# Kernel optimization log

Measured on AMD Instinct MI355X. Metric: run time of the kernel, lower is better.

Reference implementation:

```python
import jax, jax.numpy as jnp
import numpy as np

EPS = 1e-5  # torch.nn.LayerNorm default


def _layer_norm(h, g, b):
    mu = jnp.mean(h, axis=-1, keepdims=True)
    var = jnp.mean(jnp.square(h - mu), axis=-1, keepdims=True)
    return (h - mu) * jax.lax.rsqrt(var + EPS) * g + b


def setup_inputs() -> dict:
    key = jax.random.key(0)
    ks = jax.random.split(key, 16)
    N, E, D, G, H = 100000, 3200000, 16, 64, 8
    x = jax.random.normal(ks[0], (N, D), dtype=jnp.float32)
    edge_index = jax.random.randint(ks[1], (2, E), 0, N, dtype=jnp.int64)
    vp = jax.random.normal(ks[2], (G, D), dtype=jnp.float32)
    batch = jnp.sort(jax.random.randint(ks[3], (N,), 0, G, dtype=jnp.int64))
    def lin(k, fan_in, fan_out):
        bound = 1.0 / np.sqrt(fan_in)
        kw, kb = jax.random.split(k)
        W = jax.random.uniform(kw, (fan_in, fan_out), jnp.float32, -bound, bound)
        b = jax.random.uniform(kb, (fan_out,), jnp.float32, -bound, bound)
        return W, b
    W1, b1 = lin(ks[4], 3 * D, H)
    W2, b2 = lin(ks[5], H, H)
    W3, b3 = lin(ks[6], H, H)
    W4, b4 = lin(ks[7], H, 1)
    g1 = jnp.ones((H,), jnp.float32); be1 = jnp.zeros((H,), jnp.float32)
    g2 = jnp.ones((H,), jnp.float32); be2 = jnp.zeros((H,), jnp.float32)
    g3 = jnp.ones((H,), jnp.float32); be3 = jnp.zeros((H,), jnp.float32)
    return dict(x=x, edge_index=edge_index, vp=vp, batch=batch,
                W1=W1, b1=b1, g1=g1, be1=be1,
                W2=W2, b2=b2, g2=g2, be2=be2,
                W3=W3, b3=b3, g3=g3, be3=be3,
                W4=W4, b4=b4)


def reference(x, edge_index, vp, batch,
              W1, b1, g1, be1, W2, b2, g2, be2, W3, b3, g3, be3, W4, b4):
    start, end = edge_index[0], edge_index[1]
    # gather node features for both endpoints + per-graph features of the start node's event
    edge_inputs = jnp.concatenate([x[start], x[end], vp[batch[start]]], axis=1)  # [E, 3D]
    h = jnp.tanh(_layer_norm(edge_inputs @ W1 + b1, g1, be1))
    h = jnp.tanh(_layer_norm(h @ W2 + b2, g2, be2))
    h = jnp.tanh(_layer_norm(h @ W3 + b3, g3, be3))
    out = h @ W4 + b4  # [E, 1]
    return out.squeeze(-1)
```

## Files before the change

kernel.cpp:

```cpp
#include <hip/hip_runtime.h>


__device__ __forceinline__ float fast_tanh(float v) {
    float e = __expf(2.0f * v);
    return (e - 1.0f) * __builtin_amdgcn_rcpf(e + 1.0f);
}

__device__ __forceinline__ void ln_tanh8(float* h, const float* __restrict__ g,
                                         const float* __restrict__ be) {
    float mu = 0.0f;
#pragma unroll
    for (int j = 0; j < 8; ++j) mu += h[j];
    mu *= 0.125f;
    float var = 0.0f;
#pragma unroll
    for (int j = 0; j < 8; ++j) { float d = h[j] - mu; var += d * d; }
    var *= 0.125f;
    float r = __builtin_amdgcn_rsqf(var + 1e-5f);
#pragma unroll
    for (int j = 0; j < 8; ++j)
        h[j] = fast_tanh((h[j] - mu) * r * g[j] + be[j]);
}

__global__ __launch_bounds__(256) void node_pre_kernel(
    const float* __restrict__ x,
    const int* __restrict__ batch,
    const float* __restrict__ vp,
    const float* __restrict__ W1,
    const float* __restrict__ b1,
    float* __restrict__ y,
    int N)
{
    int n = blockIdx.x * blockDim.x + threadIdx.x;
    if (n >= N) return;

    const float4* px = reinterpret_cast<const float4*>(x) + (size_t)n * 4;
    float4 x0 = px[0], x1 = px[1], x2 = px[2], x3 = px[3];
    int g = batch[n];
    const float4* pv = reinterpret_cast<const float4*>(vp) + (size_t)g * 4;
    float4 v0 = pv[0], v1 = pv[1], v2 = pv[2], v3 = pv[3];

    float xs[16] = {x0.x, x0.y, x0.z, x0.w, x1.x, x1.y, x1.z, x1.w,
                    x2.x, x2.y, x2.z, x2.w, x3.x, x3.y, x3.z, x3.w};
    float vs[16] = {v0.x, v0.y, v0.z, v0.w, v1.x, v1.y, v1.z, v1.w,
                    v2.x, v2.y, v2.z, v2.w, v3.x, v3.y, v3.z, v3.w};

    float ya[8], yb[8];
#pragma unroll
    for (int j = 0; j < 8; ++j) ya[j] = b1[j];
#pragma unroll
    for (int j = 0; j < 8; ++j) yb[j] = 0.0f;

#pragma unroll
    for (int i = 0; i < 16; ++i) {
        float vx = xs[i];
        float vv = vs[i];
#pragma unroll
        for (int j = 0; j < 8; ++j) {
            ya[j] = fmaf(vx, W1[i * 8 + j], ya[j]);
            ya[j] = fmaf(vv, W1[(32 + i) * 8 + j], ya[j]);
            yb[j] = fmaf(vx, W1[(16 + i) * 8 + j], yb[j]);
        }
    }

    float4* py = reinterpret_cast<float4*>(y) + (size_t)n * 4;
    py[0] = make_float4(ya[0], ya[1], ya[2], ya[3]);
    py[1] = make_float4(ya[4], ya[5], ya[6], ya[7]);
    py[2] = make_float4(yb[0], yb[1], yb[2], yb[3]);
    py[3] = make_float4(yb[4], yb[5], yb[6], yb[7]);
}

__global__ __launch_bounds__(256) void edge_main_kernel(
    const int* __restrict__ ei,
    const float* __restrict__ y,
    const float* __restrict__ g1, const float* __restrict__ be1,
    const float* __restrict__ W2, const float* __restrict__ b2,
    const float* __restrict__ g2, const float* __restrict__ be2,
    const float* __restrict__ W3, const float* __restrict__ b3,
    const float* __restrict__ g3, const float* __restrict__ be3,
    const float* __restrict__ W4, const float* __restrict__ b4,
    float* __restrict__ out, int E)
{
    int e = blockIdx.x * blockDim.x + threadIdx.x;
    if (e >= E) return;

    int s = ei[e];
    int t = ei[E + e];

    const float4* pa = reinterpret_cast<const float4*>(y) + (size_t)s * 4;
    const float4* pb = reinterpret_cast<const float4*>(y) + (size_t)t * 4 + 2;
    float4 a0 = pa[0], a1 = pa[1];
    float4 c0 = pb[0], c1 = pb[1];

    float h[8] = {a0.x + c0.x, a0.y + c0.y, a0.z + c0.z, a0.w + c0.w,
                  a1.x + c1.x, a1.y + c1.y, a1.z + c1.z, a1.w + c1.w};
    ln_tanh8(h, g1, be1);

    float h2[8];
#pragma unroll
    for (int j = 0; j < 8; ++j) h2[j] = b2[j];
#pragma unroll
    for (int i = 0; i < 8; ++i) {
        float v = h[i];
#pragma unroll
        for (int j = 0; j < 8; ++j) h2[j] = fmaf(v, W2[i * 8 + j], h2[j]);
    }
    ln_tanh8(h2, g2, be2);

    float h3[8];
#pragma unroll
    for (int j = 0; j < 8; ++j) h3[j] = b3[j];
#pragma unroll
    for (int i = 0; i < 8; ++i) {
        float v = h2[i];
#pragma unroll
        for (int j = 0; j < 8; ++j) h3[j] = fmaf(v, W3[i * 8 + j], h3[j]);
    }
    ln_tanh8(h3, g3, be3);

    float o = b4[0];
#pragma unroll
    for (int i = 0; i < 8; ++i) o = fmaf(h3[i], W4[i], o);

    out[e] = o;
}

__global__ __launch_bounds__(256) void edge_net_fallback(
    const float* __restrict__ x, const int* __restrict__ ei,
    const float* __restrict__ vp, const int* __restrict__ batch,
    const float* __restrict__ W1, const float* __restrict__ b1,
    const float* __restrict__ g1, const float* __restrict__ be1,
    const float* __restrict__ W2, const float* __restrict__ b2,
    const float* __restrict__ g2, const float* __restrict__ be2,
    const float* __restrict__ W3, const float* __restrict__ b3,
    const float* __restrict__ g3, const float* __restrict__ be3,
    const float* __restrict__ W4, const float* __restrict__ b4,
    float* __restrict__ out, int E)
{
    int e = blockIdx.x * blockDim.x + threadIdx.x;
    if (e >= E) return;
    int s = ei[e], t = ei[E + e];
    int gb = batch[s];
    float in[48];
    const float4* ps = reinterpret_cast<const float4*>(x) + (size_t)s * 4;
    const float4* pt = reinterpret_cast<const float4*>(x) + (size_t)t * 4;
    const float4* pv = reinterpret_cast<const float4*>(vp) + (size_t)gb * 4;
#pragma unroll
    for (int q = 0; q < 4; ++q) {
        float4 a = ps[q];
        in[q*4+0]=a.x; in[q*4+1]=a.y; in[q*4+2]=a.z; in[q*4+3]=a.w;
    }
#pragma unroll
    for (int q = 0; q < 4; ++q) {
        float4 a = pt[q];
        in[16+q*4+0]=a.x; in[16+q*4+1]=a.y; in[16+q*4+2]=a.z; in[16+q*4+3]=a.w;
    }
#pragma unroll
    for (int q = 0; q < 4; ++q) {
        float4 a = pv[q];
        in[32+q*4+0]=a.x; in[32+q*4+1]=a.y; in[32+q*4+2]=a.z; in[32+q*4+3]=a.w;
    }
    float h[8];
#pragma unroll
    for (int j = 0; j < 8; ++j) h[j] = b1[j];
#pragma unroll
    for (int i = 0; i < 48; ++i) {
        float v = in[i];
#pragma unroll
        for (int j = 0; j < 8; ++j) h[j] = fmaf(v, W1[i*8+j], h[j]);
    }
    ln_tanh8(h, g1, be1);
    float h2[8];
#pragma unroll
    for (int j = 0; j < 8; ++j) h2[j] = b2[j];
#pragma unroll
    for (int i = 0; i < 8; ++i) {
        float v = h[i];
#pragma unroll
        for (int j = 0; j < 8; ++j) h2[j] = fmaf(v, W2[i*8+j], h2[j]);
    }
    ln_tanh8(h2, g2, be2);
    float h3[8];
#pragma unroll
    for (int j = 0; j < 8; ++j) h3[j] = b3[j];
#pragma unroll
    for (int i = 0; i < 8; ++i) {
        float v = h2[i];
#pragma unroll
        for (int j = 0; j < 8; ++j) h3[j] = fmaf(v, W3[i*8+j], h3[j]);
    }
    ln_tanh8(h3, g3, be3);
    float o = b4[0];
#pragma unroll
    for (int i = 0; i < 8; ++i) o = fmaf(h3[i], W4[i], o);
    out[e] = o;
}

extern "C" void kernel_launch(void* const* d_in, const int* in_sizes, int n_in,
                              void* d_out, int out_size, void* d_ws, size_t ws_size,
                              hipStream_t stream) {
    const float* x     = (const float*)d_in[0];
    const int*   ei    = (const int*)d_in[1];
    const float* vp    = (const float*)d_in[2];
    const int*   batch = (const int*)d_in[3];
    const float* W1  = (const float*)d_in[4];
    const float* b1  = (const float*)d_in[5];
    const float* g1  = (const float*)d_in[6];
    const float* be1 = (const float*)d_in[7];
    const float* W2  = (const float*)d_in[8];
    const float* b2  = (const float*)d_in[9];
    const float* g2  = (const float*)d_in[10];
    const float* be2 = (const float*)d_in[11];
    const float* W3  = (const float*)d_in[12];
    const float* b3  = (const float*)d_in[13];
    const float* g3  = (const float*)d_in[14];
    const float* be3 = (const float*)d_in[15];
    const float* W4  = (const float*)d_in[16];
    const float* b4  = (const float*)d_in[17];

    int E = in_sizes[1] / 2;
    int N = in_sizes[3];
    float* out = (float*)d_out;

    size_t y_bytes = (size_t)N * 16 * sizeof(float);
    if (ws_size >= y_bytes) {
        float* y = (float*)d_ws;
        int blockA = 256;
        int gridA = (N + blockA - 1) / blockA;
        hipLaunchKernelGGL(node_pre_kernel, dim3(gridA), dim3(blockA), 0, stream,
                           x, batch, vp, W1, b1, y, N);
        int blockB = 256;
        int gridB = (E + blockB - 1) / blockB;
        hipLaunchKernelGGL(edge_main_kernel, dim3(gridB), dim3(blockB), 0, stream,
                           ei, y, g1, be1, W2, b2, g2, be2, W3, b3, g3, be3,
                           W4, b4, out, E);
    } else {
        int block = 256;
        int grid = (E + block - 1) / block;
        hipLaunchKernelGGL(edge_net_fallback, dim3(grid), dim3(block), 0, stream,
                           x, ei, vp, batch,
                           W1, b1, g1, be1, W2, b2, g2, be2, W3, b3, g3, be3,
                           W4, b4, out, E);
    }
}
```

Before: 169.0 us.

## Store mean-centered node projections as fp16 split tables, simplify LayerNorm math

Result: faster. 149.1 us (-11.8%).

```diff
diff --git a/kernel.cpp b/kernel.cpp
--- a/kernel.cpp
+++ b/kernel.cpp
@@ -1,25 +1,11 @@
 #include <hip/hip_runtime.h>
 
+
+typedef __attribute__((ext_vector_type(8))) _Float16 h8;
 
 __device__ __forceinline__ float fast_tanh(float v) {
     float e = __expf(2.0f * v);
-    return (e - 1.0f) * __builtin_amdgcn_rcpf(e + 1.0f);
-}
-
-__device__ __forceinline__ void ln_tanh8(float* h, const float* __restrict__ g,
-                                         const float* __restrict__ be) {
-    float mu = 0.0f;
-#pragma unroll
-    for (int j = 0; j < 8; ++j) mu += h[j];
-    mu *= 0.125f;
-    float var = 0.0f;
-#pragma unroll
-    for (int j = 0; j < 8; ++j) { float d = h[j] - mu; var += d * d; }
-    var *= 0.125f;
-    float r = __builtin_amdgcn_rsqf(var + 1e-5f);
-#pragma unroll
-    for (int j = 0; j < 8; ++j)
-        h[j] = fast_tanh((h[j] - mu) * r * g[j] + be[j]);
+    return fmaf(-2.0f, __builtin_amdgcn_rcpf(e + 1.0f), 1.0f);
 }
 
 __global__ __launch_bounds__(256) void node_pre_kernel(
@@ -28,7 +14,8 @@
     const float* __restrict__ vp,
     const float* __restrict__ W1,
     const float* __restrict__ b1,
-    float* __restrict__ y,
+    h8* __restrict__ ya16,
+    h8* __restrict__ yb16,
     int N)
 {
     int n = blockIdx.x * blockDim.x + threadIdx.x;
@@ -47,9 +34,7 @@
 
     float ya[8], yb[8];
 #pragma unroll
-    for (int j = 0; j < 8; ++j) ya[j] = b1[j];
-#pragma unroll
-    for (int j = 0; j < 8; ++j) yb[j] = 0.0f;
+    for (int j = 0; j < 8; ++j) { ya[j] = b1[j]; yb[j] = 0.0f; }
 
 #pragma unroll
     for (int i = 0; i < 16; ++i) {
@@ -63,16 +48,25 @@
         }
     }
 
-    float4* py = reinterpret_cast<float4*>(y) + (size_t)n * 4;
-    py[0] = make_float4(ya[0], ya[1], ya[2], ya[3]);
-    py[1] = make_float4(ya[4], ya[5], ya[6], ya[7]);
-    py[2] = make_float4(yb[0], yb[1], yb[2], yb[3]);
-    py[3] = make_float4(yb[4], yb[5], yb[6], yb[7]);
+    float mua = 0.0f, mub = 0.0f;
+#pragma unroll
+    for (int j = 0; j < 8; ++j) { mua += ya[j]; mub += yb[j]; }
+    mua *= 0.125f; mub *= 0.125f;
+
+    h8 va, vb;
+#pragma unroll
+    for (int j = 0; j < 8; ++j) {
+        va[j] = (_Float16)(ya[j] - mua);
+        vb[j] = (_Float16)(yb[j] - mub);
+    }
+    ya16[n] = va;
+    yb16[n] = vb;
 }
 
 __global__ __launch_bounds__(256) void edge_main_kernel(
     const int* __restrict__ ei,
-    const float* __restrict__ y,
+    const h8* __restrict__ ya16,
+    const h8* __restrict__ yb16,
     const float* __restrict__ g1, const float* __restrict__ be1,
     const float* __restrict__ W2, const float* __restrict__ b2,
     const float* __restrict__ g2, const float* __restrict__ be2,
@@ -87,14 +81,20 @@
     int s = ei[e];
     int t = ei[E + e];
 
-    const float4* pa = reinterpret_cast<const float4*>(y) + (size_t)s * 4;
-    const float4* pb = reinterpret_cast<const float4*>(y) + (size_t)t * 4 + 2;
-    float4 a0 = pa[0], a1 = pa[1];
-    float4 c0 = pb[0], c1 = pb[1];
-
-    float h[8] = {a0.x + c0.x, a0.y + c0.y, a0.z + c0.z, a0.w + c0.w,
-                  a1.x + c1.x, a1.y + c1.y, a1.z + c1.z, a1.w + c1.w};
-    ln_tanh8(h, g1, be1);
+    h8 va = ya16[s];
+    h8 vb = yb16[t];
+    h8 vsum = va + vb;
+
+    float h[8];
+#pragma unroll
+    for (int j = 0; j < 8; ++j) h[j] = (float)vsum[j];
+    float ss = 0.0f;
+#pragma unroll
+    for (int j = 0; j < 8; ++j) ss = fmaf(h[j], h[j], ss);
+    float r = __builtin_amdgcn_rsqf(fmaf(ss, 0.125f, 1e-5f));
+#pragma unroll
+    for (int j = 0; j < 8; ++j)
+        h[j] = fast_tanh(fmaf(h[j], r * g1[j], be1[j]));
 
     float h2[8];
 #pragma unroll
@@ -105,7 +105,17 @@
 #pragma unroll
         for (int j = 0; j < 8; ++j) h2[j] = fmaf(v, W2[i * 8 + j], h2[j]);
     }
-    ln_tanh8(h2, g2, be2);
+    {
+        float sm = 0.0f, sq = 0.0f;
+#pragma unroll
+        for (int j = 0; j < 8; ++j) { sm += h2[j]; sq = fmaf(h2[j], h2[j], sq); }
+        float mu = sm * 0.125f;
+        float var = fmaf(sq, 0.125f, -mu * mu);
+        float rr = __builtin_amdgcn_rsqf(var + 1e-5f);
+#pragma unroll
+        for (int j = 0; j < 8; ++j)
+            h2[j] = fast_tanh(fmaf(h2[j] - mu, rr * g2[j], be2[j]));
+    }
 
     float h3[8];
 #pragma unroll
@@ -116,13 +126,36 @@
 #pragma unroll
         for (int j = 0; j < 8; ++j) h3[j] = fmaf(v, W3[i * 8 + j], h3[j]);
     }
-    ln_tanh8(h3, g3, be3);
+    {
+        float sm = 0.0f, sq = 0.0f;
+#pragma unroll
+        for (int j = 0; j < 8; ++j) { sm += h3[j]; sq = fmaf(h3[j], h3[j], sq); }
+        float mu = sm * 0.125f;
+        float var = fmaf(sq, 0.125f, -mu * mu);
+        float rr = __builtin_amdgcn_rsqf(var + 1e-5f);
+#pragma unroll
+        for (int j = 0; j < 8; ++j)
+            h3[j] = fast_tanh(fmaf(h3[j] - mu, rr * g3[j], be3[j]));
+    }
 
     float o = b4[0];
 #pragma unroll
     for (int i = 0; i < 8; ++i) o = fmaf(h3[i], W4[i], o);
 
     out[e] = o;
+}
+
+__device__ __forceinline__ void ln_tanh8_full(float* h, const float* __restrict__ g,
+                                              const float* __restrict__ be) {
+    float sm = 0.0f, sq = 0.0f;
+#pragma unroll
+    for (int j = 0; j < 8; ++j) { sm += h[j]; sq = fmaf(h[j], h[j], sq); }
+    float mu = sm * 0.125f;
+    float var = fmaf(sq, 0.125f, -mu * mu);
+    float rr = __builtin_amdgcn_rsqf(var + 1e-5f);
+#pragma unroll
+    for (int j = 0; j < 8; ++j)
+        h[j] = fast_tanh(fmaf(h[j] - mu, rr * g[j], be[j]));
 }
 
 __global__ __launch_bounds__(256) void edge_net_fallback(
@@ -169,7 +202,7 @@
 #pragma unroll
         for (int j = 0; j < 8; ++j) h[j] = fmaf(v, W1[i*8+j], h[j]);
     }
-    ln_tanh8(h, g1, be1);
+    ln_tanh8_full(h, g1, be1);
     float h2[8];
 #pragma unroll
     for (int j = 0; j < 8; ++j) h2[j] = b2[j];
@@ -179,7 +212,7 @@
 #pragma unroll
         for (int j = 0; j < 8; ++j) h2[j] = fmaf(v, W2[i*8+j], h2[j]);
     }
-    ln_tanh8(h2, g2, be2);
+    ln_tanh8_full(h2, g2, be2);
     float h3[8];
 #pragma unroll
     for (int j = 0; j < 8; ++j) h3[j] = b3[j];
@@ -189,7 +222,7 @@
 #pragma unroll
         for (int j = 0; j < 8; ++j) h3[j] = fmaf(v, W3[i*8+j], h3[j]);
     }
-    ln_tanh8(h3, g3, be3);
+    ln_tanh8_full(h3, g3, be3);
     float o = b4[0];
 #pragma unroll
     for (int i = 0; i < 8; ++i) o = fmaf(h3[i], W4[i], o);
@@ -222,18 +255,19 @@
     int N = in_sizes[3];
     float* out = (float*)d_out;
 
-    size_t y_bytes = (size_t)N * 16 * sizeof(float);
-    if (ws_size >= y_bytes) {
-        float* y = (float*)d_ws;
+    size_t tab_bytes = (size_t)N * 8 * sizeof(_Float16);
+    if (ws_size >= 2 * tab_bytes) {
+        h8* ya16 = (h8*)d_ws;
+        h8* yb16 = (h8*)((char*)d_ws + tab_bytes);
         int blockA = 256;
         int gridA = (N + blockA - 1) / blockA;
         hipLaunchKernelGGL(node_pre_kernel, dim3(gridA), dim3(blockA), 0, stream,
-                           x, batch, vp, W1, b1, y, N);
+                           x, batch, vp, W1, b1, ya16, yb16, N);
         int blockB = 256;
         int gridB = (E + blockB - 1) / blockB;
         hipLaunchKernelGGL(edge_main_kernel, dim3(gridB), dim3(blockB), 0, stream,
-                           ei, y, g1, be1, W2, b2, g2, be2, W3, b3, g3, be3,
-                           W4, b4, out, E);
+                           ei, ya16, yb16, g1, be1, W2, b2, g2, be2,
+                           W3, b3, g3, be3, W4, b4, out, E);
     } else {
         int block = 256;
         int grid = (E + block - 1) / block;
```
